# Performance work log

Measured on AMD Instinct MI355X. Metric: run time of the kernel, lower is better.

Reference implementation:

```python
import jax, jax.numpy as jnp
import numpy as np
import math

EMBED_DIM = 1024
NUM_HEADS = 16
HEAD_DIM = EMBED_DIM // NUM_HEADS
B, S = 2, 2048


def setup_inputs() -> dict:
    key = jax.random.key(0)
    ks = jax.random.split(key, 13)
    sc = 1.0 / math.sqrt(EMBED_DIM)
    inp = {
        "query": jax.random.normal(ks[0], (B, S, EMBED_DIM), jnp.float32),
        "key": jax.random.normal(ks[1], (B, S, EMBED_DIM), jnp.float32),
        "value": jax.random.normal(ks[2], (B, S, EMBED_DIM), jnp.float32),
        "input_patch_mask": jax.random.randint(ks[3], (B, S), 0, 2, jnp.int32),
        "Wq": jax.random.normal(ks[4], (EMBED_DIM, EMBED_DIM), jnp.float32) * sc,
        "bq": jnp.zeros((EMBED_DIM,), jnp.float32),
        "Wk": jax.random.normal(ks[5], (EMBED_DIM, EMBED_DIM), jnp.float32) * sc,
        "bk": jnp.zeros((EMBED_DIM,), jnp.float32),
        "Wv": jax.random.normal(ks[6], (EMBED_DIM, EMBED_DIM), jnp.float32) * sc,
        "bv": jnp.zeros((EMBED_DIM,), jnp.float32),
        "Wo": jax.random.normal(ks[7], (EMBED_DIM, EMBED_DIM), jnp.float32) * sc,
        "bo": jnp.zeros((EMBED_DIM,), jnp.float32),
    }
    return inp


def _masked_softmax(scores, mask):
    # Equivalent to masked_fill(-inf) -> softmax -> nan_to_num(0.0):
    # fully-masked rows produce exactly 0, without generating NaNs.
    neg_inf = jnp.array(-jnp.inf, scores.dtype)
    s = jnp.where(mask, scores, neg_inf)
    m = jnp.max(s, axis=-1, keepdims=True)
    m_safe = jnp.where(jnp.isfinite(m), m, jnp.zeros_like(m))
    e = jnp.where(mask, jnp.exp(s - m_safe), 0.0)
    denom = jnp.sum(e, axis=-1, keepdims=True)
    denom = jnp.where(denom == 0.0, 1.0, denom)
    return e / denom


def reference(query, key, value, input_patch_mask, Wq, bq, Wk, bk, Wv, bv, Wo, bo):
    b, s, d = query.shape
    h, hd = NUM_HEADS, HEAD_DIM
    q = (query @ Wq.T + bq).reshape(b, s, h, hd).transpose(0, 2, 1, 3)  # [b,h,s,hd]
    k = (key @ Wk.T + bk).reshape(b, s, h, hd).transpose(0, 2, 1, 3)
    v = (value @ Wv.T + bv).reshape(b, s, h, hd).transpose(0, 2, 1, 3)
    scores = jnp.einsum("bhqd,bhkd->bhqk", q, k) / math.sqrt(hd)
    # mask[b,i,j] = patch_mask[b,i] * patch_mask[b,j]
    mask = (input_patch_mask[:, :, None] * input_patch_mask[:, None, :]) > 0
    attn = _masked_softmax(scores, mask[:, None, :, :])  # dropout in eval mode = identity
    context = jnp.einsum("bhqk,bhkd->bhqd", attn, v)
    context = context.transpose(0, 2, 1, 3).reshape(b, s, d)
    return context @ Wo.T + bo
```

## Files before the change

### kernel.cpp

```cpp
#include <hip/hip_runtime.h>
#include <cstdint>
#include <cstddef>

#define EMBED 1024
#define NHEAD 16
#define HD    64
#define BATCH 2
#define SEQ   2048
#define MROWS (BATCH*SEQ)
#define QSCALE 0.1803368801111137f

typedef __bf16 bf16;
typedef __bf16 bf16x8 __attribute__((ext_vector_type(8)));
typedef float  f32x4  __attribute__((ext_vector_type(4)));
typedef unsigned int u32;

#if __has_builtin(__builtin_amdgcn_exp2f)
#define EXP2(x) __builtin_amdgcn_exp2f(x)
#else
#define EXP2(x) exp2f(x)
#endif

typedef const u32 __attribute__((address_space(1)))* gp_t;
typedef u32 __attribute__((address_space(3)))* lp_t;

__device__ __forceinline__ void g2l16(const void* g, void* l) {
  __builtin_amdgcn_global_load_lds((gp_t)(uintptr_t)g, (lp_t)(u32)(uintptr_t)l, 16, 0, 0);
}

#define MFMA(a, b, c) __builtin_amdgcn_mfma_f32_16x16x32_bf16((a), (b), (c), 0, 0, 0)

#define SZX8 ((MROWS*EMBED)/8)
#define SZW8 ((EMBED*EMBED)/8)

__global__ void cast_all(const float* __restrict__ q, const float* __restrict__ k,
                         const float* __restrict__ v, const float* __restrict__ wq,
                         const float* __restrict__ wk, const float* __restrict__ wv,
                         const float* __restrict__ wo,
                         bf16* xq, bf16* xk, bf16* xv,
                         bf16* wqb, bf16* wkb, bf16* wvb, bf16* wob) {
  int z = blockIdx.y;
  const float* in; bf16* out;
  switch (z) {
    case 0: in = q;  out = xq;  break;
    case 1: in = k;  out = xk;  break;
    case 2: in = v;  out = xv;  break;
    case 3: in = wq; out = wqb; break;
    case 4: in = wk; out = wkb; break;
    case 5: in = wv; out = wvb; break;
    default: in = wo; out = wob; break;
  }
  int n8 = (z < 3) ? SZX8 : SZW8;
  int i = blockIdx.x * blockDim.x + threadIdx.x;
  if (i >= n8) return;
  const float4* p = (const float4*)in;
  float4 a = p[2*i], b = p[2*i+1];
  union { bf16 h[8]; uint4 u; } r;
  r.h[0] = (bf16)a.x; r.h[1] = (bf16)a.y; r.h[2] = (bf16)a.z; r.h[3] = (bf16)a.w;
  r.h[4] = (bf16)b.x; r.h[5] = (bf16)b.y; r.h[6] = (bf16)b.z; r.h[7] = (bf16)b.w;
  ((uint4*)out)[i] = r.u;
}

#define BM 128
#define BN 128
#define BK 32
#define NKI (EMBED/BK)

__device__ __forceinline__ void gemm_core(
    const bf16* __restrict__ A, const bf16* __restrict__ W,
    int m0, int n0, bf16* Al, bf16* Bl, f32x4 (&acc)[4][4])
{
  const int tid  = threadIdx.x;
  const int lane = tid & 63, wid = tid >> 6;
  const int quad = lane >> 4, l16 = lane & 15;
  const int wm = wid >> 1, wn = wid & 1;

  const int R = tid >> 2, Cc = tid & 3;
  const int gcol = (Cc ^ ((R >> 1) & 3)) * 8;
  const bf16* Ag = A + (size_t)(m0 + R) * EMBED + gcol;
  const bf16* Bg = W + (size_t)(n0 + R) * EMBED + gcol;
  bf16* AlW = Al + wid * 512;
  bf16* BlW = Bl + wid * 512;

  g2l16(Ag, AlW);                      g2l16(Ag + (size_t)64*EMBED, AlW + 2048);
  g2l16(Bg, BlW);                      g2l16(Bg + (size_t)64*EMBED, BlW + 2048);
  __syncthreads();

  for (int ki = 0; ki < NKI; ++ki) {
    const int cur = ki & 1;
    if (ki + 1 < NKI) {
      const int nb = cur ^ 1;
      const int k0 = (ki + 1) * BK;
      g2l16(Ag + k0, AlW + nb*4096);
      g2l16(Ag + (size_t)64*EMBED + k0, AlW + nb*4096 + 2048);
      g2l16(Bg + k0, BlW + nb*4096);
      g2l16(Bg + (size_t)64*EMBED + k0, BlW + nb*4096 + 2048);
    }
    const bf16* Ac = Al + cur*4096;
    const bf16* Bc = Bl + cur*4096;
    bf16x8 af[4], bg[4];
#pragma unroll
    for (int i = 0; i < 4; ++i) {
      int ra = wm*64 + i*16 + l16;
      af[i] = *(const bf16x8*)(Ac + ra*32 + ((quad ^ ((ra>>1)&3))*8));
      int rb = wn*64 + i*16 + l16;
      bg[i] = *(const bf16x8*)(Bc + rb*32 + ((quad ^ ((rb>>1)&3))*8));
    }
#pragma unroll
    for (int i = 0; i < 4; ++i)
#pragma unroll
      for (int j = 0; j < 4; ++j)
        acc[i][j] = MFMA(af[i], bg[j], acc[i][j]);
    __syncthreads();
  }
}

__global__ __launch_bounds__(256) void qkv_kernel(
    const bf16* __restrict__ Xq, const bf16* __restrict__ Xk, const bf16* __restrict__ Xv,
    const bf16* __restrict__ Wq, const bf16* __restrict__ Wk, const bf16* __restrict__ Wv,
    const float* __restrict__ bq, const float* __restrict__ bk, const float* __restrict__ bv,
    bf16* __restrict__ Qp, bf16* __restrict__ Kp, bf16* __restrict__ VTg)
{
  __shared__ bf16 Al[2*BM*BK];
  __shared__ bf16 Bl[2*BN*BK];
  const int z = blockIdx.z;
  const bf16* A = z==0 ? Xq : z==1 ? Xk : Wv;
  const bf16* W = z==0 ? Wq : z==1 ? Wk : Xv;
  const float* bias = z==0 ? bq : z==1 ? bk : bv;
  const float scale = (z==0) ? QSCALE : 1.0f;
  const int m0 = (z < 2) ? blockIdx.y * BM : blockIdx.x * BM;
  const int n0 = (z < 2) ? blockIdx.x * BN : blockIdx.y * BN;

  f32x4 acc[4][4] = {};
  gemm_core(A, W, m0, n0, Al, Bl, acc);

  const int lane = threadIdx.x & 63, wid = threadIdx.x >> 6;
  const int quad = lane >> 4, l16 = lane & 15;
  const int wm = wid >> 1, wn = wid & 1;

#pragma unroll
  for (int i = 0; i < 4; ++i) {
#pragma unroll
    for (int j = 0; j < 4; ++j) {
      int col = n0 + wn*64 + j*16 + l16;
      if (z < 2) {
        float bv2 = bias[col];
        bf16* outp = (z == 0) ? Qp : Kp;
#pragma unroll
        for (int r = 0; r < 4; ++r) {
          int row = m0 + wm*64 + i*16 + quad*4 + r;
          outp[(size_t)row*EMBED + col] = (bf16)((acc[i][j][r] + bv2) * scale);
        }
      } else {
        int t  = col;
        int bb = t >> 11, ss = t & (SEQ-1);
        int tile = ss >> 6;
        int ppos = l16*4 + (j & 3);
#pragma unroll
        for (int r = 0; r < 4; ++r) {
          int e = m0 + wm*64 + i*16 + quad*4 + r;
          int hh = e >> 6, dd = e & (HD-1);
          VTg[(((size_t)bb*NHEAD + hh)*HD + dd)*SEQ + tile*64 + ppos]
              = (bf16)(acc[i][j][r] + bias[e]);
        }
      }
    }
  }
}

__global__ __launch_bounds__(256) void oproj_kernel(
    const bf16* __restrict__ Ctx, const bf16* __restrict__ Wo,
    const float* __restrict__ bo, float* __restrict__ out)
{
  __shared__ bf16 Al[2*128*32];
  __shared__ bf16 Bl[2*64*32];
  const int tid  = threadIdx.x;
  const int lane = tid & 63, wid = tid >> 6;
  const int quad = lane >> 4, l16 = lane & 15;
  const int m0 = blockIdx.y * 128, n0 = blockIdx.x * 64;

  const int R = tid >> 2, Cc = tid & 3;
  const int gcol = (Cc ^ ((R >> 1) & 3)) * 8;
  const bf16* Ag = Ctx + (size_t)(m0 + R) * EMBED + gcol;
  const bf16* Bg = Wo  + (size_t)(n0 + R) * EMBED + gcol;
  bf16* AlW = Al + wid * 512;
  bf16* BlW = Bl + wid * 512;

  g2l16(Ag, AlW);  g2l16(Ag + (size_t)64*EMBED, AlW + 2048);
  g2l16(Bg, BlW);
  __syncthreads();

  f32x4 acc[2][4] = {};
  for (int ki = 0; ki < NKI; ++ki) {
    const int cur = ki & 1;
    if (ki + 1 < NKI) {
      const int nb = cur ^ 1;
      const int k0 = (ki + 1) * BK;
      g2l16(Ag + k0, AlW + nb*4096);
      g2l16(Ag + (size_t)64*EMBED + k0, AlW + nb*4096 + 2048);
      g2l16(Bg + k0, BlW + nb*2048);
    }
    const bf16* Ac = Al + cur*4096;
    const bf16* Bc = Bl + cur*2048;
    bf16x8 af[2], bg[4];
#pragma unroll
    for (int u = 0; u < 2; ++u) {
      int ra = wid*32 + u*16 + l16;
      af[u] = *(const bf16x8*)(Ac + ra*32 + ((quad ^ ((ra>>1)&3))*8));
    }
#pragma unroll
    for (int j = 0; j < 4; ++j) {
      int rb = j*16 + l16;
      bg[j] = *(const bf16x8*)(Bc + rb*32 + ((quad ^ ((rb>>1)&3))*8));
    }
#pragma unroll
    for (int u = 0; u < 2; ++u)
#pragma unroll
      for (int j = 0; j < 4; ++j)
        acc[u][j] = MFMA(af[u], bg[j], acc[u][j]);
    __syncthreads();
  }

#pragma unroll
  for (int u = 0; u < 2; ++u)
#pragma unroll
    for (int j = 0; j < 4; ++j) {
      int col = n0 + j*16 + l16;
      float bv = bo[col];
#pragma unroll
      for (int r = 0; r < 4; ++r) {
        int row = m0 + wid*32 + u*16 + quad*4 + r;
        out[(size_t)row*EMBED + col] = (acc[u][j][r] + bv);
      }
    }
}

#define NT  (SEQ/64)
#define PST 72

__global__ __launch_bounds__(256, 2) void attn_kernel(
    const bf16* __restrict__ Qp, const bf16* __restrict__ Kp, const bf16* __restrict__ VT,
    const int* __restrict__ pmask, bf16* __restrict__ Ctx)
{
  __shared__ __align__(16) bf16 Kt[2][64*64];
  __shared__ __align__(16) bf16 Vt[2][64*64];
  __shared__ __align__(16) bf16 Pl[2][4][32*PST];
  __shared__ float Mb[SEQ];

  const int qt = blockIdx.x, h = blockIdx.y, b = blockIdx.z;
  const int tid = threadIdx.x, lane = tid & 63, wid = tid >> 6;
  const int quad = lane >> 4, l16 = lane & 15;
  const int qrow0 = qt*128 + wid*32;

  {
    int i = tid * 8;
    const int4* pm4 = (const int4*)(pmask + b*SEQ + i);
    int4 a = pm4[0], c = pm4[1];
    float4 f0, f1;
    f0.x = a.x ? 0.f : -1e30f;  f0.y = a.y ? 0.f : -1e30f;
    f0.z = a.z ? 0.f : -1e30f;  f0.w = a.w ? 0.f : -1e30f;
    f1.x = c.x ? 0.f : -1e30f;  f1.y = c.y ? 0.f : -1e30f;
    f1.z = c.z ? 0.f : -1e30f;  f1.w = c.w ? 0.f : -1e30f;
    *(float4*)(Mb + i)     = f0;
    *(float4*)(Mb + i + 4) = f1;
  }

  bf16x8 qf[2][2];
#pragma unroll
  for (int u = 0; u < 2; ++u) {
    const size_t qoff = (size_t)(b*SEQ + qrow0 + u*16 + l16)*EMBED + h*HD;
    qf[u][0] = *(const bf16x8*)(Qp + qoff + quad*8);
    qf[u][1] = *(const bf16x8*)(Qp + qoff + 32 + quad*8);
  }

  int qm[2][4];
#pragma unroll
  for (int u = 0; u < 2; ++u)
#pragma unroll
    for (int r = 0; r < 4; ++r) qm[u][r] = pmask[b*SEQ + qrow0 + u*16 + quad*4 + r];

  bf16 onev = (bf16)1.0f;
  bf16x8 ones = {onev, onev, onev, onev, onev, onev, onev, onev};

  const bf16* Kg  = Kp + (size_t)b*SEQ*EMBED + h*HD;
  const bf16* VTg = VT + (size_t)(b*NHEAD + h)*HD*SEQ;

  const int R = tid >> 3;
  const int Cc = tid & 7;
  const int scol = (Cc ^ (R & 7)) * 8;

  f32x4 o[2][4] = {};
  f32x4 lacc[2] = {};

#define STAGE_K(kt, buf) do {                                                \
    const bf16* kg = Kg + (size_t)((kt)*64 + R)*EMBED + scol;                \
    bf16* kl = &Kt[buf][0] + wid*512;                                        \
    g2l16(kg, kl);  g2l16(kg + (size_t)32*EMBED, kl + 2048);                 \
  } while (0)
#define STAGE_V(kt, buf) do {                                                \
    const bf16* vg = VTg + (size_t)R*SEQ + (kt)*64 + scol;                   \
    bf16* vl = &Vt[buf][0] + wid*512;                                        \
    g2l16(vg, vl);  g2l16(vg + (size_t)32*SEQ, vl + 2048);                   \
  } while (0)

  STAGE_K(0, 0);
  __syncthreads();

#pragma unroll 2
  for (int kt = 0; kt < NT; ++kt) {
    const int cur = kt & 1;
    if (kt + 1 < NT) STAGE_K(kt + 1, cur ^ 1);
    STAGE_V(kt, cur);

    const bf16* Kc = &Kt[cur][0];
    f32x4 sg[2][4];
#pragma unroll
    for (int g = 0; g < 4; ++g) {
      int ra = g*16 + l16, sa = ra & 7;
      bf16x8 kfa = *(const bf16x8*)(Kc + ra*64 + ((quad     ^ sa)*8));
      bf16x8 kfb = *(const bf16x8*)(Kc + ra*64 + (((quad+4) ^ sa)*8));
#pragma unroll
      for (int u = 0; u < 2; ++u) {
        f32x4 s = {};
        s = MFMA(qf[u][0], kfa, s);
        s = MFMA(qf[u][1], kfb, s);
        sg[u][g] = s;
      }
    }

    if (kt > 0) {
      const bf16* Vc = &Vt[cur ^ 1][0];
      bf16x8 pf[2][2];
#pragma unroll
      for (int u = 0; u < 2; ++u) {
        const bf16* Pw = &Pl[cur ^ 1][wid][u*16*PST];
        pf[u][0] = *(const bf16x8*)(Pw + l16*PST + quad*8);
        pf[u][1] = *(const bf16x8*)(Pw + l16*PST + 32 + quad*8);
        lacc[u] = MFMA(pf[u][0], ones, lacc[u]);
        lacc[u] = MFMA(pf[u][1], ones, lacc[u]);
      }
#pragma unroll
      for (int t = 0; t < 4; ++t) {
        int rd = t*16 + l16, sd = rd & 7;
        bf16x8 vf0 = *(const bf16x8*)(Vc + rd*64 + ((quad     ^ sd)*8));
        bf16x8 vf1 = *(const bf16x8*)(Vc + rd*64 + (((quad+4) ^ sd)*8));
#pragma unroll
        for (int u = 0; u < 2; ++u) {
          o[u][t] = MFMA(pf[u][0], vf0, o[u][t]);
          o[u][t] = MFMA(pf[u][1], vf1, o[u][t]);
        }
      }
    }

    float bias[4];
#pragma unroll
    for (int g = 0; g < 4; ++g) bias[g] = Mb[kt*64 + g*16 + l16];
#pragma unroll
    for (int u = 0; u < 2; ++u) {
      bf16* Pw = &Pl[cur][wid][u*16*PST];
#pragma unroll
      for (int r = 0; r < 4; ++r) {
        union { bf16 h[4]; uint2 uu; } pk;
#pragma unroll
        for (int g = 0; g < 4; ++g) pk.h[g] = (bf16)EXP2(sg[u][g][r] + bias[g]);
        *(uint2*)(Pw + (quad*4 + r)*PST + l16*4) = pk.uu;
      }
    }
    __syncthreads();
  }

  {
    const bf16* Vc = &Vt[(NT - 1) & 1][0];
    bf16x8 pf[2][2];
#pragma unroll
    for (int u = 0; u < 2; ++u) {
      const bf16* Pw = &Pl[(NT - 1) & 1][wid][u*16*PST];
      pf[u][0] = *(const bf16x8*)(Pw + l16*PST + quad*8);
      pf[u][1] = *(const bf16x8*)(Pw + l16*PST + 32 + quad*8);
      lacc[u] = MFMA(pf[u][0], ones, lacc[u]);
      lacc[u] = MFMA(pf[u][1], ones, lacc[u]);
    }
#pragma unroll
    for (int t = 0; t < 4; ++t) {
      int rd = t*16 + l16, sd = rd & 7;
      bf16x8 vf0 = *(const bf16x8*)(Vc + rd*64 + ((quad     ^ sd)*8));
      bf16x8 vf1 = *(const bf16x8*)(Vc + rd*64 + (((quad+4) ^ sd)*8));
#pragma unroll
      for (int u = 0; u < 2; ++u) {
        o[u][t] = MFMA(pf[u][0], vf0, o[u][t]);
        o[u][t] = MFMA(pf[u][1], vf1, o[u][t]);
      }
    }
  }

#pragma unroll
  for (int u = 0; u < 2; ++u) {
    float inv[4];
#pragma unroll
    for (int r = 0; r < 4; ++r)
      inv[r] = (qm[u][r] && lacc[u][r] > 0.f) ? 1.0f / lacc[u][r] : 0.0f;
#pragma unroll
    for (int t = 0; t < 4; ++t)
#pragma unroll
      for (int r = 0; r < 4; ++r) {
        int row = b*SEQ + qrow0 + u*16 + quad*4 + r;
        Ctx[(size_t)row*EMBED + h*HD + t*16 + l16] = (bf16)(o[u][t][r] * inv[r]);
      }
  }
}

extern "C" void kernel_launch(void* const* d_in, const int* in_sizes, int n_in,
                              void* d_out, int out_size, void* d_ws, size_t ws_size,
                              hipStream_t stream)
{
  const float* query = (const float*)d_in[0];
  const float* key   = (const float*)d_in[1];
  const float* value = (const float*)d_in[2];
  const int*   pm    = (const int*)d_in[3];
  const float* Wq = (const float*)d_in[4];
  const float* bq = (const float*)d_in[5];
  const float* Wk = (const float*)d_in[6];
  const float* bk = (const float*)d_in[7];
  const float* Wv = (const float*)d_in[8];
  const float* bv = (const float*)d_in[9];
  const float* Wo = (const float*)d_in[10];
  const float* bo = (const float*)d_in[11];
  float* out = (float*)d_out;

  const size_t SZ_X = (size_t)MROWS * EMBED;
  const size_t SZ_W = (size_t)EMBED * EMBED;

  bf16* p   = (bf16*)d_ws;
  bf16* Xq  = p; p += SZ_X;
  bf16* Xk  = p; p += SZ_X;
  bf16* Xv  = p; p += SZ_X;
  bf16* Wqb = p; p += SZ_W;
  bf16* Wkb = p; p += SZ_W;
  bf16* Wvb = p; p += SZ_W;
  bf16* Wob = p; p += SZ_W;
  bf16* Qp  = p; p += SZ_X;
  bf16* Kp  = p; p += SZ_X;
  bf16* VTg = p; p += SZ_X;
  bf16* Ctx = p; p += SZ_X;

  dim3 gc((unsigned)(SZX8/256), 7);
  cast_all<<<gc, 256, 0, stream>>>(query, key, value, Wq, Wk, Wv, Wo,
                                   Xq, Xk, Xv, Wqb, Wkb, Wvb, Wob);

  dim3 gq(EMBED/BN, MROWS/BM, 3);
  qkv_kernel<<<gq, 256, 0, stream>>>(Xq, Xk, Xv, Wqb, Wkb, Wvb, bq, bk, bv, Qp, Kp, VTg);

  dim3 ga(SEQ/128, NHEAD, BATCH);
  attn_kernel<<<ga, 256, 0, stream>>>(Qp, Kp, VTg, pm, Ctx);

  dim3 gg(EMBED/64, MROWS/128);
  oproj_kernel<<<gg, 256, 0, stream>>>(Ctx, Wob, bo, out);
}
```

Measured before the change: 225.9 us.

## Fuse fp32-to-bf16 casts into GEMM loaders and single-buffer attention P tile

```diff
diff --git a/kernel.cpp b/kernel.cpp
--- a/kernel.cpp
+++ b/kernel.cpp
@@ -30,35 +30,11 @@
 
 #define MFMA(a, b, c) __builtin_amdgcn_mfma_f32_16x16x32_bf16((a), (b), (c), 0, 0, 0)
 
-#define SZX8 ((MROWS*EMBED)/8)
-#define SZW8 ((EMBED*EMBED)/8)
-
-__global__ void cast_all(const float* __restrict__ q, const float* __restrict__ k,
-                         const float* __restrict__ v, const float* __restrict__ wq,
-                         const float* __restrict__ wk, const float* __restrict__ wv,
-                         const float* __restrict__ wo,
-                         bf16* xq, bf16* xk, bf16* xv,
-                         bf16* wqb, bf16* wkb, bf16* wvb, bf16* wob) {
-  int z = blockIdx.y;
-  const float* in; bf16* out;
-  switch (z) {
-    case 0: in = q;  out = xq;  break;
-    case 1: in = k;  out = xk;  break;
-    case 2: in = v;  out = xv;  break;
-    case 3: in = wq; out = wqb; break;
-    case 4: in = wk; out = wkb; break;
-    case 5: in = wv; out = wvb; break;
-    default: in = wo; out = wob; break;
-  }
-  int n8 = (z < 3) ? SZX8 : SZW8;
-  int i = blockIdx.x * blockDim.x + threadIdx.x;
-  if (i >= n8) return;
-  const float4* p = (const float4*)in;
-  float4 a = p[2*i], b = p[2*i+1];
+__device__ __forceinline__ uint4 cvt8(float4 a, float4 b) {
   union { bf16 h[8]; uint4 u; } r;
   r.h[0] = (bf16)a.x; r.h[1] = (bf16)a.y; r.h[2] = (bf16)a.z; r.h[3] = (bf16)a.w;
   r.h[4] = (bf16)b.x; r.h[5] = (bf16)b.y; r.h[6] = (bf16)b.z; r.h[7] = (bf16)b.w;
-  ((uint4*)out)[i] = r.u;
+  return r.u;
 }
 
 #define BM 128
@@ -66,8 +42,8 @@
 #define BK 32
 #define NKI (EMBED/BK)
 
-__device__ __forceinline__ void gemm_core(
-    const bf16* __restrict__ A, const bf16* __restrict__ W,
+__device__ __forceinline__ void gemm_core_f32(
+    const float* __restrict__ A, const float* __restrict__ W,
     int m0, int n0, bf16* Al, bf16* Bl, f32x4 (&acc)[4][4])
 {
   const int tid  = threadIdx.x;
@@ -77,24 +53,34 @@
 
   const int R = tid >> 2, Cc = tid & 3;
   const int gcol = (Cc ^ ((R >> 1) & 3)) * 8;
-  const bf16* Ag = A + (size_t)(m0 + R) * EMBED + gcol;
-  const bf16* Bg = W + (size_t)(n0 + R) * EMBED + gcol;
-  bf16* AlW = Al + wid * 512;
-  bf16* BlW = Bl + wid * 512;
-
-  g2l16(Ag, AlW);                      g2l16(Ag + (size_t)64*EMBED, AlW + 2048);
-  g2l16(Bg, BlW);                      g2l16(Bg + (size_t)64*EMBED, BlW + 2048);
+  const float* Ag = A + (size_t)(m0 + R) * EMBED + gcol;
+  const float* Bg = W + (size_t)(n0 + R) * EMBED + gcol;
+  const int dst = R*32 + Cc*8;
+
+  {
+    float4 a0 = *(const float4*)(Ag),                    a1 = *(const float4*)(Ag + 4);
+    float4 a2 = *(const float4*)(Ag + (size_t)64*EMBED), a3 = *(const float4*)(Ag + (size_t)64*EMBED + 4);
+    float4 b0 = *(const float4*)(Bg),                    b1 = *(const float4*)(Bg + 4);
+    float4 b2 = *(const float4*)(Bg + (size_t)64*EMBED), b3 = *(const float4*)(Bg + (size_t)64*EMBED + 4);
+    *(uint4*)(Al + dst)        = cvt8(a0, a1);
+    *(uint4*)(Al + dst + 2048) = cvt8(a2, a3);
+    *(uint4*)(Bl + dst)        = cvt8(b0, b1);
+    *(uint4*)(Bl + dst + 2048) = cvt8(b2, b3);
+  }
   __syncthreads();
 
   for (int ki = 0; ki < NKI; ++ki) {
     const int cur = ki & 1;
-    if (ki + 1 < NKI) {
-      const int nb = cur ^ 1;
+    float4 a0, a1, a2, a3, b0, b1, b2, b3;
+    const bool pre = (ki + 1 < NKI);
+    if (pre) {
       const int k0 = (ki + 1) * BK;
-      g2l16(Ag + k0, AlW + nb*4096);
-      g2l16(Ag + (size_t)64*EMBED + k0, AlW + nb*4096 + 2048);
-      g2l16(Bg + k0, BlW + nb*4096);
-      g2l16(Bg + (size_t)64*EMBED + k0, BlW + nb*4096 + 2048);
+      a0 = *(const float4*)(Ag + k0);  a1 = *(const float4*)(Ag + k0 + 4);
+      a2 = *(const float4*)(Ag + (size_t)64*EMBED + k0);
+      a3 = *(const float4*)(Ag + (size_t)64*EMBED + k0 + 4);
+      b0 = *(const float4*)(Bg + k0);  b1 = *(const float4*)(Bg + k0 + 4);
+      b2 = *(const float4*)(Bg + (size_t)64*EMBED + k0);
+      b3 = *(const float4*)(Bg + (size_t)64*EMBED + k0 + 4);
     }
     const bf16* Ac = Al + cur*4096;
     const bf16* Bc = Bl + cur*4096;
@@ -111,28 +97,35 @@
 #pragma unroll
       for (int j = 0; j < 4; ++j)
         acc[i][j] = MFMA(af[i], bg[j], acc[i][j]);
+    if (pre) {
+      const int nb = cur ^ 1;
+      *(uint4*)(Al + nb*4096 + dst)        = cvt8(a0, a1);
+      *(uint4*)(Al + nb*4096 + dst + 2048) = cvt8(a2, a3);
+      *(uint4*)(Bl + nb*4096 + dst)        = cvt8(b0, b1);
+      *(uint4*)(Bl + nb*4096 + dst + 2048) = cvt8(b2, b3);
+    }
     __syncthreads();
   }
 }
 
 __global__ __launch_bounds__(256) void qkv_kernel(
-    const bf16* __restrict__ Xq, const bf16* __restrict__ Xk, const bf16* __restrict__ Xv,
-    const bf16* __restrict__ Wq, const bf16* __restrict__ Wk, const bf16* __restrict__ Wv,
+    const float* __restrict__ Xq, const float* __restrict__ Xk, const float* __restrict__ Xv,
+    const float* __restrict__ Wq, const float* __restrict__ Wk, const float* __restrict__ Wv,
     const float* __restrict__ bq, const float* __restrict__ bk, const float* __restrict__ bv,
     bf16* __restrict__ Qp, bf16* __restrict__ Kp, bf16* __restrict__ VTg)
 {
   __shared__ bf16 Al[2*BM*BK];
   __shared__ bf16 Bl[2*BN*BK];
   const int z = blockIdx.z;
-  const bf16* A = z==0 ? Xq : z==1 ? Xk : Wv;
-  const bf16* W = z==0 ? Wq : z==1 ? Wk : Xv;
+  const float* A = z==0 ? Xq : z==1 ? Xk : Wv;
+  const float* W = z==0 ? Wq : z==1 ? Wk : Xv;
   const float* bias = z==0 ? bq : z==1 ? bk : bv;
   const float scale = (z==0) ? QSCALE : 1.0f;
   const int m0 = (z < 2) ? blockIdx.y * BM : blockIdx.x * BM;
   const int n0 = (z < 2) ? blockIdx.x * BN : blockIdx.y * BN;
 
   f32x4 acc[4][4] = {};
-  gemm_core(A, W, m0, n0, Al, Bl, acc);
+  gemm_core_f32(A, W, m0, n0, Al, Bl, acc);
 
   const int lane = threadIdx.x & 63, wid = threadIdx.x >> 6;
   const int quad = lane >> 4, l16 = lane & 15;
@@ -169,7 +162,7 @@
 }
 
 __global__ __launch_bounds__(256) void oproj_kernel(
-    const bf16* __restrict__ Ctx, const bf16* __restrict__ Wo,
+    const bf16* __restrict__ Ctx, const float* __restrict__ Wo,
     const float* __restrict__ bo, float* __restrict__ out)
 {
   __shared__ bf16 Al[2*128*32];
@@ -181,24 +174,29 @@
 
   const int R = tid >> 2, Cc = tid & 3;
   const int gcol = (Cc ^ ((R >> 1) & 3)) * 8;
-  const bf16* Ag = Ctx + (size_t)(m0 + R) * EMBED + gcol;
-  const bf16* Bg = Wo  + (size_t)(n0 + R) * EMBED + gcol;
+  const bf16*  Ag = Ctx + (size_t)(m0 + R) * EMBED + gcol;
+  const float* Bg = Wo  + (size_t)(n0 + R) * EMBED + gcol;
   bf16* AlW = Al + wid * 512;
-  bf16* BlW = Bl + wid * 512;
+  const int dst = R*32 + Cc*8;
 
   g2l16(Ag, AlW);  g2l16(Ag + (size_t)64*EMBED, AlW + 2048);
-  g2l16(Bg, BlW);
+  {
+    float4 b0 = *(const float4*)(Bg), b1 = *(const float4*)(Bg + 4);
+    *(uint4*)(Bl + dst) = cvt8(b0, b1);
+  }
   __syncthreads();
 
   f32x4 acc[2][4] = {};
   for (int ki = 0; ki < NKI; ++ki) {
     const int cur = ki & 1;
-    if (ki + 1 < NKI) {
+    float4 b0, b1;
+    const bool pre = (ki + 1 < NKI);
+    if (pre) {
       const int nb = cur ^ 1;
       const int k0 = (ki + 1) * BK;
       g2l16(Ag + k0, AlW + nb*4096);
       g2l16(Ag + (size_t)64*EMBED + k0, AlW + nb*4096 + 2048);
-      g2l16(Bg + k0, BlW + nb*2048);
+      b0 = *(const float4*)(Bg + k0);  b1 = *(const float4*)(Bg + k0 + 4);
     }
     const bf16* Ac = Al + cur*4096;
     const bf16* Bc = Bl + cur*2048;
@@ -218,6 +216,7 @@
 #pragma unroll
       for (int j = 0; j < 4; ++j)
         acc[u][j] = MFMA(af[u], bg[j], acc[u][j]);
+    if (pre) *(uint4*)(Bl + (cur^1)*2048 + dst) = cvt8(b0, b1);
     __syncthreads();
   }
 
@@ -244,7 +243,7 @@
 {
   __shared__ __align__(16) bf16 Kt[2][64*64];
   __shared__ __align__(16) bf16 Vt[2][64*64];
-  __shared__ __align__(16) bf16 Pl[2][4][32*PST];
+  __shared__ __align__(16) bf16 Pl[4][32*PST];
   __shared__ float Mb[SEQ];
 
   const int qt = blockIdx.x, h = blockIdx.y, b = blockIdx.z;
@@ -333,7 +332,7 @@
       bf16x8 pf[2][2];
 #pragma unroll
       for (int u = 0; u < 2; ++u) {
-        const bf16* Pw = &Pl[cur ^ 1][wid][u*16*PST];
+        const bf16* Pw = &Pl[wid][u*16*PST];
         pf[u][0] = *(const bf16x8*)(Pw + l16*PST + quad*8);
         pf[u][1] = *(const bf16x8*)(Pw + l16*PST + 32 + quad*8);
         lacc[u] = MFMA(pf[u][0], ones, lacc[u]);
@@ -357,7 +356,7 @@
     for (int g = 0; g < 4; ++g) bias[g] = Mb[kt*64 + g*16 + l16];
 #pragma unroll
     for (int u = 0; u < 2; ++u) {
-      bf16* Pw = &Pl[cur][wid][u*16*PST];
+      bf16* Pw = &Pl[wid][u*16*PST];
 #pragma unroll
       for (int r = 0; r < 4; ++r) {
         union { bf16 h[4]; uint2 uu; } pk;
@@ -374,7 +373,7 @@
     bf16x8 pf[2][2];
 #pragma unroll
     for (int u = 0; u < 2; ++u) {
-      const bf16* Pw = &Pl[(NT - 1) & 1][wid][u*16*PST];
+      const bf16* Pw = &Pl[wid][u*16*PST];
       pf[u][0] = *(const bf16x8*)(Pw + l16*PST + quad*8);
       pf[u][1] = *(const bf16x8*)(Pw + l16*PST + 32 + quad*8);
       lacc[u] = MFMA(pf[u][0], ones, lacc[u]);
@@ -428,31 +427,19 @@
   float* out = (float*)d_out;
 
   const size_t SZ_X = (size_t)MROWS * EMBED;
-  const size_t SZ_W = (size_t)EMBED * EMBED;
 
   bf16* p   = (bf16*)d_ws;
-  bf16* Xq  = p; p += SZ_X;
-  bf16* Xk  = p; p += SZ_X;
-  bf16* Xv  = p; p += SZ_X;
-  bf16* Wqb = p; p += SZ_W;
-  bf16* Wkb = p; p += SZ_W;
-  bf16* Wvb = p; p += SZ_W;
-  bf16* Wob = p; p += SZ_W;
   bf16* Qp  = p; p += SZ_X;
   bf16* Kp  = p; p += SZ_X;
   bf16* VTg = p; p += SZ_X;
   bf16* Ctx = p; p += SZ_X;
 
-  dim3 gc((unsigned)(SZX8/256), 7);
-  cast_all<<<gc, 256, 0, stream>>>(query, key, value, Wq, Wk, Wv, Wo,
-                                   Xq, Xk, Xv, Wqb, Wkb, Wvb, Wob);
-
   dim3 gq(EMBED/BN, MROWS/BM, 3);
-  qkv_kernel<<<gq, 256, 0, stream>>>(Xq, Xk, Xv, Wqb, Wkb, Wvb, bq, bk, bv, Qp, Kp, VTg);
+  qkv_kernel<<<gq, 256, 0, stream>>>(query, key, value, Wq, Wk, Wv, bq, bk, bv, Qp, Kp, VTg);
 
   dim3 ga(SEQ/128, NHEAD, BATCH);
   attn_kernel<<<ga, 256, 0, stream>>>(Qp, Kp, VTg, pm, Ctx);
 
   dim3 gg(EMBED/64, MROWS/128);
-  oproj_kernel<<<gg, 256, 0, stream>>>(Ctx, Wob, bo, out);
-}
+  oproj_kernel<<<gg, 256, 0, stream>>>(Ctx, Wo, bo, out);
+}
```

Result: slower. 242.7 us (+7.4%).
